# Kernel tuning notes

Hardware: AMD Instinct MI355X
Metric: run time of the kernel (lower is better)

Reference implementation:

```python
import jax, jax.numpy as jnp
import numpy as np

N = 25000          # nodes
E = 400000         # edges (avg degree 16)
H = 64             # hidden_nf
TYPE_DIM = 1
NL = 5             # 4 gcl layers + dgcl_0 (identical shapes, stacked)
GROUP = jnp.array([[[1., 0.], [0., 1.]], [[-1., 0.], [0., -1.]]], dtype=jnp.float32)  # [G,2,2]


def setup_inputs() -> dict:
    key = jax.random.key(0)
    ks = iter(jax.random.split(key, 40))
    def nrm(shape, scale=0.05):
        return jax.random.normal(next(ks), shape, dtype=jnp.float32) * scale
    inp = {}
    inp["nodes"] = nrm((N, 4 + TYPE_DIM), 1.0)
    inp["edges"] = jax.random.randint(next(ks), (2, E), 0, N)
    inp["edge_attr"] = nrm((E, 1), 1.0)
    # embedding: Linear(input_dim, H)
    inp["W_emb"] = nrm((4 + TYPE_DIM, H)); inp["b_emb"] = jnp.zeros((H,), jnp.float32)
    # group_mlp: Linear(G*H, H) -> SiLU -> Linear(H, H)
    G = GROUP.shape[0]
    inp["Wg1"] = nrm((G * H, H)); inp["bg1"] = jnp.zeros((H,), jnp.float32)
    inp["Wg2"] = nrm((H, H));     inp["bg2"] = jnp.zeros((H,), jnp.float32)
    # stacked GCL params for gcl_0..3 + dgcl_0 (all H->H, edges_in_nf=1)
    inp["eW1"] = nrm((NL, 2 * H + 1, H)); inp["eb1"] = jnp.zeros((NL, H), jnp.float32)
    inp["eW2"] = nrm((NL, H, H));         inp["eb2"] = jnp.zeros((NL, H), jnp.float32)
    inp["nW1"] = nrm((NL, 2 * H, H));     inp["nb1"] = jnp.zeros((NL, H), jnp.float32)
    inp["nW2"] = nrm((NL, H, H));         inp["nb2"] = jnp.zeros((NL, H), jnp.float32)
    # dgcl_1: GCL(H, 2*len(group)=4, H)
    inp["deW1"] = nrm((2 * H + 1, H)); inp["deb1"] = jnp.zeros((H,), jnp.float32)
    inp["deW2"] = nrm((H, H));         inp["deb2"] = jnp.zeros((H,), jnp.float32)
    inp["dnW1"] = nrm((2 * H, H));     inp["dnb1"] = jnp.zeros((H,), jnp.float32)
    inp["dnW2"] = nrm((H, 2 * G));     inp["dnb2"] = jnp.zeros((2 * G,), jnp.float32)
    return inp


def _gcl(h, row, col, edge_attr, eW1, eb1, eW2, eb2, nW1, nb1, nW2, nb2):
    # edge model: gather -> MLP (Linear,SiLU,Linear,SiLU)
    e_in = jnp.concatenate([h[row], h[col], edge_attr], axis=1)  # [E, 2H+1]
    e = jax.nn.silu(e_in @ eW1 + eb1)
    e = jax.nn.silu(e @ eW2 + eb2)                               # [E, H]
    # node model: scatter-sum by source index, then MLP (Linear,SiLU,Linear)
    agg = jax.ops.segment_sum(e, row, num_segments=h.shape[0])   # [N, H]
    out = jnp.concatenate([h, agg], axis=1)                      # [N, 2H]
    out = jax.nn.silu(out @ nW1 + nb1) @ nW2 + nb2
    return out  # recurrent=False: no residual


def reference(nodes, edges, edge_attr, W_emb, b_emb, Wg1, bg1, Wg2, bg2,
              eW1, eb1, eW2, eb2, nW1, nb1, nW2, nb2,
              deW1, deb1, deW2, deb2, dnW1, dnb1, dnW2, dnb2):
    loc, vel, ntype = nodes[:, :2], nodes[:, 2:4], nodes[:, 4:]
    # group-equivariant embedding: transform loc/vel by each group element
    loc_g = jnp.einsum('nd,gde->gne', loc, GROUP)   # [G, N, 2]
    vel_g = jnp.einsum('nd,gde->gne', vel, GROUP)   # [G, N, 2]
    ntype_g = jnp.broadcast_to(ntype, (GROUP.shape[0],) + ntype.shape)
    feats = jnp.concatenate([loc_g, vel_g, ntype_g], axis=2)   # [G, N, 5]
    h_g = feats @ W_emb + b_emb                                 # [G, N, H]
    h = jnp.transpose(h_g, (1, 0, 2)).reshape(nodes.shape[0], -1)  # [N, G*H]
    h = jax.nn.silu(h @ Wg1 + bg1) @ Wg2 + bg2
    row, col = edges[0], edges[1]
    for i in range(eW1.shape[0]):  # gcl_0..3 then dgcl_0
        h = _gcl(h, row, col, edge_attr, eW1[i], eb1[i], eW2[i], eb2[i],
                 nW1[i], nb1[i], nW2[i], nb2[i])
    # dgcl_1: node output dim = 2*len(group)
    x = _gcl(h, row, col, edge_attr, deW1, deb1, deW2, deb2,
             dnW1, dnb1, dnW2, dnb2)
    return x
```

## Files before the change

kernel.cpp:

```cpp
#include <hip/hip_runtime.h>
#include <hip/hip_bf16.h>

#define N_NODES 25000
#define N_EDGES 400000
#define NB_SCAN ((N_NODES + 255) / 256)
#define EDGE_TILES (N_EDGES / 16)
#define TPW 2
#define EDGE_WAVES (EDGE_TILES / TPW)
#define EDGE_BLOCKS (EDGE_WAVES / 4)
#define NODE_TILES ((N_NODES + 15) / 16)
#define NODE_BLOCKS2 ((NODE_TILES + 1) / 2)

typedef __attribute__((ext_vector_type(8))) short short8;
typedef __attribute__((ext_vector_type(4))) float f32x4;

__device__ __forceinline__ float silu_f(float x) {
  return x * __builtin_amdgcn_rcpf(1.0f + __expf(-x));
}

__device__ __forceinline__ short f2bf_s(float x) {
  __hip_bfloat16 h = __float2bfloat16(x);
  return *reinterpret_cast<short*>(&h);
}
__device__ __forceinline__ float bf_s2f(short s) {
  __hip_bfloat16 h = *reinterpret_cast<__hip_bfloat16*>(&s);
  return __bfloat162float(h);
}

__device__ __forceinline__ void load_afrag(const float* T, int s, int quad, int n16,
                                           short8& ahi, short8& alo) {
#pragma unroll
  for (int j = 0; j < 8; ++j) {
    float tv = T[(s * 32 + quad * 8 + j) * 17 + n16];
    short hi = f2bf_s(tv);
    ahi[j] = hi;
    alo[j] = f2bf_s(tv - bf_s2f(hi));
  }
}
__device__ __forceinline__ void load_bfrag(const float* __restrict__ W, int k0, int col,
                                           short8& bhi, short8& blo) {
#pragma unroll
  for (int j = 0; j < 8; ++j) {
    float w = W[(k0 + j) * 64 + col];
    short hi = f2bf_s(w);
    bhi[j] = hi;
    blo[j] = f2bf_s(w - bf_s2f(hi));
  }
}
__device__ __forceinline__ f32x4 mfma3(short8 ahi, short8 alo, short8 bhi, short8 blo,
                                       f32x4 acc) {
  acc = __builtin_amdgcn_mfma_f32_16x16x32_bf16(ahi, bhi, acc, 0, 0, 0);
  acc = __builtin_amdgcn_mfma_f32_16x16x32_bf16(ahi, blo, acc, 0, 0, 0);
  acc = __builtin_amdgcn_mfma_f32_16x16x32_bf16(alo, bhi, acc, 0, 0, 0);
  return acc;
}

__global__ __launch_bounds__(256) void k_hist(const int* __restrict__ rows,
                                              int* __restrict__ counts)
{
  int stride = gridDim.x * blockDim.x;
  for (int e = blockIdx.x * blockDim.x + threadIdx.x; e < N_EDGES; e += stride)
    atomicAdd(&counts[rows[e]], 1);
}

__global__ __launch_bounds__(256) void k_scanA(const int* __restrict__ counts,
                                               int* __restrict__ bsum)
{
  __shared__ int sd[256];
  int t = threadIdx.x;
  int i = blockIdx.x * 256 + t;
  int x = (i < N_NODES) ? counts[i] : 0;
  sd[t] = x; __syncthreads();
  for (int d = 128; d > 0; d >>= 1) { if (t < d) sd[t] += sd[t + d]; __syncthreads(); }
  if (t == 0) bsum[blockIdx.x] = sd[0];
}

__global__ __launch_bounds__(128) void k_scanB(const int* __restrict__ bsum,
                                               int* __restrict__ boffs)
{
  __shared__ int buf[128];
  int t = threadIdx.x;
  int x = (t < NB_SCAN) ? bsum[t] : 0;
  buf[t] = x; __syncthreads();
  for (int d = 1; d < 128; d <<= 1) {
    int y = (t >= d) ? buf[t - d] : 0;
    __syncthreads();
    buf[t] += y;
    __syncthreads();
  }
  if (t < NB_SCAN) boffs[t] = buf[t] - x;
}

__global__ __launch_bounds__(256) void k_scanC(const int* __restrict__ counts,
                                               const int* __restrict__ boffs,
                                               int* __restrict__ cursor)
{
  __shared__ int buf[256];
  int t = threadIdx.x;
  int i = blockIdx.x * 256 + t;
  int x = (i < N_NODES) ? counts[i] : 0;
  buf[t] = x; __syncthreads();
  for (int d = 1; d < 256; d <<= 1) {
    int y = (t >= d) ? buf[t - d] : 0;
    __syncthreads();
    buf[t] += y;
    __syncthreads();
  }
  if (i < N_NODES) cursor[i] = boffs[blockIdx.x] + buf[t] - x;
}

__global__ __launch_bounds__(256) void k_scatter(
    const int* __restrict__ rows, const int* __restrict__ cols,
    const float* __restrict__ eatt, int* __restrict__ cursor,
    int* __restrict__ srow, int* __restrict__ scol, float* __restrict__ sea)
{
  int stride = gridDim.x * blockDim.x;
  for (int e = blockIdx.x * blockDim.x + threadIdx.x; e < N_EDGES; e += stride) {
    int r = rows[e];
    int pos = atomicAdd(&cursor[r], 1);
    srow[pos] = r;
    scol[pos] = cols[e];
    sea[pos] = eatt[e];
  }
}

__global__ __launch_bounds__(256) void k_w2prep(const float* __restrict__ eW2,
                                                const float* __restrict__ deW2,
                                                short* __restrict__ w2p)
{
  int layer = blockIdx.x;
  const float* src = (layer < 5) ? (eW2 + layer * 64 * 64) : deW2;
  short* dst = w2p + layer * 8192;
  for (int t = threadIdx.x; t < 4096; t += 256) {
    int j = t & 7, n16 = (t >> 3) & 15, quad = (t >> 7) & 3, nt = (t >> 9) & 3,
        s = (t >> 11) & 1;
    float val = src[(s * 32 + quad * 8 + j) * 64 + nt * 16 + n16];
    short hi = f2bf_s(val);
    short lo = f2bf_s(val - bf_s2f(hi));
    int base = ((s * 4 + nt) * 4 + quad) * 128 + n16 * 8 + j;
    dst[base] = hi;
    dst[base + 4096] = lo;
  }
}

__global__ __launch_bounds__(256, 2) void k_embed_fused(
    const float* __restrict__ nodes,
    const float* __restrict__ W_emb, const float* __restrict__ b_emb,
    const float* __restrict__ Wg1, const float* __restrict__ bg1,
    const float* __restrict__ Wg2, const float* __restrict__ bg2,
    const float* __restrict__ eW1_0, const float* __restrict__ eb1_0,
    float* __restrict__ h, float* __restrict__ u, float* __restrict__ v,
    float* __restrict__ agg)
{
  const int lane = threadIdx.x & 63;
  const int wv = threadIdx.x >> 6;
  const int n16 = lane & 15;
  const int quad = lane >> 4;
  const int col = wv * 16 + n16;

  short8 W1hi[4], W1lo[4], W2hi[2], W2lo[2], Uhi[2], Ulo[2], Vhi[2], Vlo[2];
#pragma unroll
  for (int s = 0; s < 4; ++s)
    load_bfrag(Wg1, s * 32 + quad * 8, col, W1hi[s], W1lo[s]);
#pragma unroll
  for (int s = 0; s < 2; ++s) {
    load_bfrag(Wg2, s * 32 + quad * 8, col, W2hi[s], W2lo[s]);
    load_bfrag(eW1_0, s * 32 + quad * 8, col, Uhi[s], Ulo[s]);
    load_bfrag(eW1_0 + 64 * 64, s * 32 + quad * 8, col, Vhi[s], Vlo[s]);
  }
  float bg1v = bg1[col], bg2v = bg2[col], ebv = eb1_0[col];
  float w0 = W_emb[0 * 64 + lane], w1 = W_emb[1 * 64 + lane],
        w2 = W_emb[2 * 64 + lane], w3 = W_emb[3 * 64 + lane],
        w4 = W_emb[4 * 64 + lane];
  float bev = b_emb[lane];

  __shared__ float Ta[128 * 17];
  __shared__ float Tt[64 * 17];
  __shared__ float Th[64 * 17];
  __shared__ float Tu[64 * 17];
  __shared__ float Tv[64 * 17];

  int n0 = blockIdx.x * 16;
#pragma unroll
  for (int e4 = 0; e4 < 4; ++e4) {
    int e = wv * 4 + e4;
    int n = min(n0 + e, N_NODES - 1);
    float x0 = nodes[n * 5 + 0], x1 = nodes[n * 5 + 1],
          x2 = nodes[n * 5 + 2], x3 = nodes[n * 5 + 3],
          x4 = nodes[n * 5 + 4];
    float base = bev + x4 * w4;
    float sv = x0 * w0 + x1 * w1 + x2 * w2 + x3 * w3;
    Ta[lane * 17 + e] = base + sv;
    Ta[(64 + lane) * 17 + e] = base - sv;
  }
  __syncthreads();

  f32x4 a1 = {};
#pragma unroll
  for (int s = 0; s < 4; ++s) {
    short8 ahi, alo;
    load_afrag(Ta, s, quad, n16, ahi, alo);
    a1 = mfma3(ahi, alo, W1hi[s], W1lo[s], a1);
  }
#pragma unroll
  for (int r = 0; r < 4; ++r)
    Tt[col * 17 + quad * 4 + r] = silu_f(a1[r] + bg1v);
  __syncthreads();

  f32x4 a2 = {};
#pragma unroll
  for (int s = 0; s < 2; ++s) {
    short8 ahi, alo;
    load_afrag(Tt, s, quad, n16, ahi, alo);
    a2 = mfma3(ahi, alo, W2hi[s], W2lo[s], a2);
  }
#pragma unroll
  for (int r = 0; r < 4; ++r)
    Th[col * 17 + quad * 4 + r] = a2[r] + bg2v;
  __syncthreads();

  f32x4 aU = {}, aV = {};
#pragma unroll
  for (int s = 0; s < 2; ++s) {
    short8 ahi, alo;
    load_afrag(Th, s, quad, n16, ahi, alo);
    aU = mfma3(ahi, alo, Uhi[s], Ulo[s], aU);
    aV = mfma3(ahi, alo, Vhi[s], Vlo[s], aV);
  }
#pragma unroll
  for (int r = 0; r < 4; ++r) {
    Tu[col * 17 + quad * 4 + r] = aU[r] + ebv;
    Tv[col * 17 + quad * 4 + r] = aV[r];
  }
  __syncthreads();

#pragma unroll
  for (int e4 = 0; e4 < 4; ++e4) {
    int e = wv * 4 + e4;
    int n = n0 + e;
    if (n < N_NODES) {
      h[n * 64 + lane] = Th[lane * 17 + e];
      u[n * 64 + lane] = Tu[lane * 17 + e];
      v[n * 64 + lane] = Tv[lane * 17 + e];
      agg[n * 64 + lane] = 0.f;
    }
  }
}

__global__ __launch_bounds__(256, 2) void k_postfused(
    float* __restrict__ h, float* __restrict__ agg,
    const float* __restrict__ nW1, const float* __restrict__ nb1,
    const float* __restrict__ nW2, const float* __restrict__ nb2,
    const float* __restrict__ eW1n, const float* __restrict__ eb1n,
    float* __restrict__ u, float* __restrict__ v)
{
  const int lane = threadIdx.x & 63;
  const int wv = threadIdx.x >> 6;
  const int n16 = lane & 15;
  const int quad = lane >> 4;
  const int col = wv * 16 + n16;

  short8 W1hi[4], W1lo[4], W2hi[2], W2lo[2], Uhi[2], Ulo[2], Vhi[2], Vlo[2];
#pragma unroll
  for (int s = 0; s < 4; ++s)
    load_bfrag(nW1, s * 32 + quad * 8, col, W1hi[s], W1lo[s]);
#pragma unroll
  for (int s = 0; s < 2; ++s) {
    load_bfrag(nW2, s * 32 + quad * 8, col, W2hi[s], W2lo[s]);
    load_bfrag(eW1n, s * 32 + quad * 8, col, Uhi[s], Ulo[s]);
    load_bfrag(eW1n + 64 * 64, s * 32 + quad * 8, col, Vhi[s], Vlo[s]);
  }
  float b1 = nb1[col], b2 = nb2[col], ebv = eb1n[col];

  __shared__ float LA[2][128 * 17];
  __shared__ float LB[2][64 * 17];

  int t0 = blockIdx.x * 2;
#pragma unroll
  for (int q = 0; q < 2; ++q) {
    int n0 = (t0 + q) * 16;
#pragma unroll
    for (int e4 = 0; e4 < 4; ++e4) {
      int e = wv * 4 + e4;
      int n = min(n0 + e, N_NODES - 1);
      LA[q][lane * 17 + e] = h[n * 64 + lane];
      LA[q][(64 + lane) * 17 + e] = agg[n * 64 + lane];
    }
  }
  __syncthreads();

  f32x4 a1[2] = {};
#pragma unroll
  for (int q = 0; q < 2; ++q)
#pragma unroll
    for (int s = 0; s < 4; ++s) {
      short8 ahi, alo;
      load_afrag(LA[q], s, quad, n16, ahi, alo);
      a1[q] = mfma3(ahi, alo, W1hi[s], W1lo[s], a1[q]);
    }
#pragma unroll
  for (int q = 0; q < 2; ++q)
#pragma unroll
    for (int r = 0; r < 4; ++r)
      LB[q][col * 17 + quad * 4 + r] = silu_f(a1[q][r] + b1);
  __syncthreads();

  f32x4 a2[2] = {};
#pragma unroll
  for (int q = 0; q < 2; ++q)
#pragma unroll
    for (int s = 0; s < 2; ++s) {
      short8 ahi, alo;
      load_afrag(LB[q], s, quad, n16, ahi, alo);
      a2[q] = mfma3(ahi, alo, W2hi[s], W2lo[s], a2[q]);
    }
#pragma unroll
  for (int q = 0; q < 2; ++q)
#pragma unroll
    for (int r = 0; r < 4; ++r)
      LA[q][col * 17 + quad * 4 + r] = a2[q][r] + b2;
  __syncthreads();

  f32x4 aU[2] = {}, aV[2] = {};
#pragma unroll
  for (int q = 0; q < 2; ++q)
#pragma unroll
    for (int s = 0; s < 2; ++s) {
      short8 ahi, alo;
      load_afrag(LA[q], s, quad, n16, ahi, alo);
      aU[q] = mfma3(ahi, alo, Uhi[s], Ulo[s], aU[q]);
      aV[q] = mfma3(ahi, alo, Vhi[s], Vlo[s], aV[q]);
    }
#pragma unroll
  for (int q = 0; q < 2; ++q)
#pragma unroll
    for (int r = 0; r < 4; ++r) {
      LA[q][1088 + col * 17 + quad * 4 + r] = aU[q][r] + ebv;
      LB[q][col * 17 + quad * 4 + r] = aV[q][r];
    }
  __syncthreads();

#pragma unroll
  for (int q = 0; q < 2; ++q) {
    int n0 = (t0 + q) * 16;
#pragma unroll
    for (int e4 = 0; e4 < 4; ++e4) {
      int e = wv * 4 + e4;
      int n = n0 + e;
      if (n < N_NODES) {
        h[n * 64 + lane] = LA[q][lane * 17 + e];
        u[n * 64 + lane] = LA[q][1088 + lane * 17 + e];
        v[n * 64 + lane] = LB[q][lane * 17 + e];
        agg[n * 64 + lane] = 0.f;
      }
    }
  }
}

__global__ __launch_bounds__(256) void k_edge(
    const float* __restrict__ u, const float* __restrict__ v,
    const int* __restrict__ srow, const int* __restrict__ scol,
    const float* __restrict__ sea,
    const float* __restrict__ wea,
    const short* __restrict__ w2p, const float* __restrict__ eb2,
    float* __restrict__ agg)
{
  const int lane = threadIdx.x & 63;
  const int wv = threadIdx.x >> 6;
  const int n16 = lane & 15;
  const int quad = lane >> 4;

  const int wid = blockIdx.x * 4 + wv;
  const int tile0 = wid * TPW;
  int e0 = tile0 * 16;
  int e1 = e0 + 16;
  int rA = srow[e0 + n16], cA = scol[e0 + n16];
  int rB = srow[e1 + n16], cB = scol[e1 + n16];
  float eaA = sea[e0 + n16];
  float eaB = sea[e1 + n16];

  float4 weq[4];
  weq[0] = *reinterpret_cast<const float4*>(&wea[quad * 8]);
  weq[1] = *reinterpret_cast<const float4*>(&wea[quad * 8 + 4]);
  weq[2] = *reinterpret_cast<const float4*>(&wea[32 + quad * 8]);
  weq[3] = *reinterpret_cast<const float4*>(&wea[32 + quad * 8 + 4]);
  float b2v[4];
#pragma unroll
  for (int nt = 0; nt < 4; ++nt) b2v[nt] = eb2[nt * 16 + n16];

  auto gather_frag = [&](int r, int c, float4 (&uu)[4], float4 (&vv)[4]) {
    const float* ub = u + r * 64 + quad * 8;
    const float* vb = v + c * 64 + quad * 8;
    uu[0] = *reinterpret_cast<const float4*>(ub);
    uu[1] = *reinterpret_cast<const float4*>(ub + 4);
    uu[2] = *reinterpret_cast<const float4*>(ub + 32);
    uu[3] = *reinterpret_cast<const float4*>(ub + 36);
    vv[0] = *reinterpret_cast<const float4*>(vb);
    vv[1] = *reinterpret_cast<const float4*>(vb + 4);
    vv[2] = *reinterpret_cast<const float4*>(vb + 32);
    vv[3] = *reinterpret_cast<const float4*>(vb + 36);
  };

  float4 uuA[4], vvA[4];
  gather_frag(rA, cA, uuA, vvA);

  const short8* Wp8 = reinterpret_cast<const short8*>(w2p);
  short8 Whi[2][4], Wlo[2][4];
#pragma unroll
  for (int s = 0; s < 2; ++s)
#pragma unroll
    for (int nt = 0; nt < 4; ++nt) {
      Whi[s][nt] = Wp8[((s * 4 + nt) * 4 + quad) * 16 + n16];
      Wlo[s][nt] = Wp8[((s * 4 + nt) * 4 + quad) * 16 + n16 + 512];
    }

  int cur_row = -1;
  bool first_atomic = true;
  float asum[4] = {0.f, 0.f, 0.f, 0.f};

  auto reduce_pick = [&](float a0, float a1, float a2, float a3) -> float {
    a0 += __shfl_xor(a0, 16); a0 += __shfl_xor(a0, 32);
    a1 += __shfl_xor(a1, 16); a1 += __shfl_xor(a1, 32);
    a2 += __shfl_xor(a2, 16); a2 += __shfl_xor(a2, 32);
    a3 += __shfl_xor(a3, 16); a3 += __shfl_xor(a3, 32);
    float o = a0;
    o = (quad == 1) ? a1 : o;
    o = (quad == 2) ? a2 : o;
    o = (quad == 3) ? a3 : o;
    return o;
  };

  auto make_frags = [&](const float4 (&uu)[4], const float4 (&vv)[4], float ea,
                        short8 (&ahi)[2], short8 (&alo)[2]) {
    const float* uf = reinterpret_cast<const float*>(uu);
    const float* vf = reinterpret_cast<const float*>(vv);
    const float* wf = reinterpret_cast<const float*>(weq);
#pragma unroll
    for (int k = 0; k < 16; ++k) {
      float t = silu_f(uf[k] + vf[k] + ea * wf[k]);
      short hi = f2bf_s(t);
      ahi[k >> 3][k & 7] = hi;
      alo[k >> 3][k & 7] = f2bf_s(t - bf_s2f(hi));
    }
  };

  auto do_mfma = [&](const short8 (&ahi)[2], const short8 (&alo)[2], f32x4 (&acc)[4]) {
#pragma unroll
    for (int s = 0; s < 2; ++s)
#pragma unroll
      for (int nt = 0; nt < 4; ++nt) {
        acc[nt] = __builtin_amdgcn_mfma_f32_16x16x32_bf16(ahi[s], Whi[s][nt], acc[nt], 0, 0, 0);
        acc[nt] = __builtin_amdgcn_mfma_f32_16x16x32_bf16(ahi[s], Wlo[s][nt], acc[nt], 0, 0, 0);
        acc[nt] = __builtin_amdgcn_mfma_f32_16x16x32_bf16(alo[s], Whi[s][nt], acc[nt], 0, 0, 0);
      }
  };

  auto epilogue = [&](int r16a, f32x4 (&acc)[4]) {
    float ev[4][4];
#pragma unroll
    for (int reg = 0; reg < 4; ++reg)
#pragma unroll
      for (int nt = 0; nt < 4; ++nt)
        ev[reg][nt] = silu_f(acc[nt][reg] + b2v[nt]);

    int rup = __shfl_up(r16a, 1);
    bool nf = (lane < 16) && ((lane == 0) ? (r16a != cur_row) : (r16a != rup));
    unsigned mask = (unsigned)(__ballot(nf) & 0xFFFFull);

    int s = 0;
    while (s < 16) {
      if ((mask >> s) & 1u) {
        if (cur_row >= 0) {
          float o = reduce_pick(asum[0], asum[1], asum[2], asum[3]);
          if (first_atomic) { unsafeAtomicAdd(&agg[cur_row * 64 + lane], o); first_atomic = false; }
          else agg[cur_row * 64 + lane] = o;
        }
        asum[0] = asum[1] = asum[2] = asum[3] = 0.f;
        cur_row = __shfl(r16a, s);
      }
      unsigned rem = mask & ~((2u << s) - 1u);
      int e = rem ? (__ffs(rem) - 1) : 16;
#pragma unroll
      for (int reg = 0; reg < 4; ++reg) {
        int m = quad * 4 + reg;
        bool in = (m >= s) && (m < e);
        asum[0] += in ? ev[reg][0] : 0.f;
        asum[1] += in ? ev[reg][1] : 0.f;
        asum[2] += in ? ev[reg][2] : 0.f;
        asum[3] += in ? ev[reg][3] : 0.f;
      }
      s = e;
    }
  };

  short8 ahiA[2], aloA[2];
  make_frags(uuA, vvA, eaA, ahiA, aloA);
  float4 uuB[4], vvB[4];
  gather_frag(rB, cB, uuB, vvB);
  f32x4 accA[4] = {};
  do_mfma(ahiA, aloA, accA);
  epilogue(rA, accA);

  short8 ahiB[2], aloB[2];
  make_frags(uuB, vvB, eaB, ahiB, aloB);
  f32x4 accB[4] = {};
  do_mfma(ahiB, aloB, accB);
  epilogue(rB, accB);

  if (cur_row >= 0) {
    float o = reduce_pick(asum[0], asum[1], asum[2], asum[3]);
    unsafeAtomicAdd(&agg[cur_row * 64 + lane], o);
  }
}

__global__ __launch_bounds__(256, 2) void k_final_mfma(
    const float* __restrict__ h, const float* __restrict__ agg,
    const float* __restrict__ dnW1, const float* __restrict__ dnb1,
    const float* __restrict__ dnW2, const float* __restrict__ dnb2,
    float* __restrict__ out)
{
  const int lane = threadIdx.x & 63;
  const int wv = threadIdx.x >> 6;
  const int n16 = lane & 15;
  const int quad = lane >> 4;
  const int col = wv * 16 + n16;

  short8 W1hi[4], W1lo[4];
#pragma unroll
  for (int s = 0; s < 4; ++s)
    load_bfrag(dnW1, s * 32 + quad * 8, col, W1hi[s], W1lo[s]);
  float b1 = dnb1[col];

  __shared__ float Ta[128 * 17];
  __shared__ float Tt[64 * 17];
  __shared__ float W2s[256];
  __shared__ float Tp[4][64];

  W2s[threadIdx.x] = dnW2[threadIdx.x];

  int n0 = blockIdx.x * 16;
#pragma unroll
  for (int e4 = 0; e4 < 4; ++e4) {
    int e = wv * 4 + e4;
    int n = min(n0 + e, N_NODES - 1);
    Ta[lane * 17 + e] = h[n * 64 + lane];
    Ta[(64 + lane) * 17 + e] = agg[n * 64 + lane];
  }
  __syncthreads();

  f32x4 a1 = {};
#pragma unroll
  for (int s = 0; s < 4; ++s) {
    short8 ahi, alo;
    load_afrag(Ta, s, quad, n16, ahi, alo);
    a1 = mfma3(ahi, alo, W1hi[s], W1lo[s], a1);
  }
#pragma unroll
  for (int r = 0; r < 4; ++r)
    Tt[col * 17 + quad * 4 + r] = silu_f(a1[r] + b1);
  __syncthreads();

  int m = lane >> 2, c = lane & 3;
  float p = 0.f;
#pragma unroll
  for (int kk = 0; kk < 16; ++kk) {
    int k = wv * 16 + kk;
    p += Tt[k * 17 + m] * W2s[k * 4 + c];
  }
  Tp[wv][lane] = p;
  __syncthreads();

  if (threadIdx.x < 64) {
    int n = n0 + (threadIdx.x >> 2);
    if (n < N_NODES) {
      float o = Tp[0][threadIdx.x] + Tp[1][threadIdx.x] +
                Tp[2][threadIdx.x] + Tp[3][threadIdx.x] + dnb2[threadIdx.x & 3];
      out[n * 4 + (threadIdx.x & 3)] = o;
    }
  }
}

extern "C" void kernel_launch(void* const* d_in, const int* in_sizes, int n_in,
                              void* d_out, int out_size, void* d_ws, size_t ws_size,
                              hipStream_t stream)
{
  const float* nodes = (const float*)d_in[0];
  const int*   edges = (const int*)d_in[1];
  const float* eatt  = (const float*)d_in[2];
  const float* W_emb = (const float*)d_in[3];
  const float* b_emb = (const float*)d_in[4];
  const float* Wg1   = (const float*)d_in[5];
  const float* bg1   = (const float*)d_in[6];
  const float* Wg2   = (const float*)d_in[7];
  const float* bg2   = (const float*)d_in[8];
  const float* eW1   = (const float*)d_in[9];
  const float* eb1   = (const float*)d_in[10];
  const float* eW2   = (const float*)d_in[11];
  const float* eb2   = (const float*)d_in[12];
  const float* nW1   = (const float*)d_in[13];
  const float* nb1   = (const float*)d_in[14];
  const float* nW2   = (const float*)d_in[15];
  const float* nb2   = (const float*)d_in[16];
  const float* deW1  = (const float*)d_in[17];
  const float* deb1  = (const float*)d_in[18];
  const float* deW2  = (const float*)d_in[19];
  const float* deb2  = (const float*)d_in[20];
  const float* dnW1  = (const float*)d_in[21];
  const float* dnb1  = (const float*)d_in[22];
  const float* dnW2  = (const float*)d_in[23];
  const float* dnb2  = (const float*)d_in[24];
  float* out = (float*)d_out;

  float* h   = (float*)d_ws;
  float* u   = h + N_NODES * 64;
  float* v   = u + N_NODES * 64;
  float* agg = v + N_NODES * 64;
  int* counts = (int*)(agg + N_NODES * 64);
  int* cursor = counts + N_NODES;
  int* bsum   = cursor + N_NODES;
  int* boffs  = bsum + 128;
  int* srow   = boffs + 128;
  int* scol   = srow + N_EDGES;
  float* sea  = (float*)(scol + N_EDGES);
  short* w2p  = (short*)(sea + N_EDGES);

  const int* rows = edges;
  const int* cols = edges + N_EDGES;

  hipMemsetAsync(counts, 0, N_NODES * sizeof(int), stream);
  k_w2prep<<<6, 256, 0, stream>>>(eW2, deW2, w2p);
  k_hist<<<400, 256, 0, stream>>>(rows, counts);
  k_scanA<<<NB_SCAN, 256, 0, stream>>>(counts, bsum);
  k_scanB<<<1, 128, 0, stream>>>(bsum, boffs);
  k_scanC<<<NB_SCAN, 256, 0, stream>>>(counts, boffs, cursor);
  k_scatter<<<400, 256, 0, stream>>>(rows, cols, eatt, cursor, srow, scol, sea);

  k_embed_fused<<<NODE_TILES, 256, 0, stream>>>(nodes, W_emb, b_emb, Wg1, bg1,
                                                Wg2, bg2, eW1, eb1, h, u, v, agg);

  for (int i = 0; i < 5; ++i) {
    k_edge<<<EDGE_BLOCKS, 256, 0, stream>>>(u, v, srow, scol, sea,
                                            eW1 + i * 129 * 64 + 128 * 64,
                                            w2p + i * 8192, eb2 + i * 64, agg);
    const float* eW1next = (i < 4) ? (eW1 + (i + 1) * 129 * 64) : deW1;
    const float* eb1next = (i < 4) ? (eb1 + (i + 1) * 64) : deb1;
    k_postfused<<<NODE_BLOCKS2, 256, 0, stream>>>(h, agg,
                                                  nW1 + i * 128 * 64, nb1 + i * 64,
                                                  nW2 + i * 64 * 64, nb2 + i * 64,
                                                  eW1next, eb1next, u, v);
  }
  k_edge<<<EDGE_BLOCKS, 256, 0, stream>>>(u, v, srow, scol, sea, deW1 + 128 * 64,
                                          w2p + 5 * 8192, deb2, agg);
  k_final_mfma<<<NODE_TILES, 256, 0, stream>>>(h, agg, dnW1, dnb1, dnW2, dnb2, out);
}
```

Baseline: 508.0 us.

## Stage edge-MLP weights in LDS and raise k_edge occupancy target

The edge kernel now copies the packed bf16 second-layer weights and edge-attr weights into shared memory once per block and reads the MFMA B fragments from LDS inside the loop. Before, each lane held them in registers. The two edge tiles are processed in a sequential loop rather than a manually software-pipelined A/B schedule, and launch bounds request 8 blocks per CU. The aim is to cut register pressure so more waves can hide gather latency. In exchange it adds LDS traffic, a block barrier, and loses the explicit overlap of the second tile's gather with the first tile's compute.

Result: faster. 447.3 us (-11.9%).

```diff
diff --git a/kernel.cpp b/kernel.cpp
--- a/kernel.cpp
+++ b/kernel.cpp
@@ -357,7 +357,7 @@
   }
 }
 
-__global__ __launch_bounds__(256) void k_edge(
+__global__ __launch_bounds__(256, 8) void k_edge(
     const float* __restrict__ u, const float* __restrict__ v,
     const int* __restrict__ srow, const int* __restrict__ scol,
     const float* __restrict__ sea,
@@ -370,49 +370,25 @@
   const int n16 = lane & 15;
   const int quad = lane >> 4;
 
+  __shared__ short Wlds[8192];
+  __shared__ float weqlds[64];
+
+  {
+    const int4* s4 = reinterpret_cast<const int4*>(w2p);
+    int4* d4 = reinterpret_cast<int4*>(Wlds);
+    for (int i = threadIdx.x; i < 1024; i += 256) d4[i] = s4[i];
+    if (threadIdx.x < 64) weqlds[threadIdx.x] = wea[threadIdx.x];
+  }
+  __syncthreads();
+
+  const short8* WL = reinterpret_cast<const short8*>(Wlds);
+
+  float b2v[4];
+#pragma unroll
+  for (int nt = 0; nt < 4; ++nt) b2v[nt] = eb2[nt * 16 + n16];
+
   const int wid = blockIdx.x * 4 + wv;
   const int tile0 = wid * TPW;
-  int e0 = tile0 * 16;
-  int e1 = e0 + 16;
-  int rA = srow[e0 + n16], cA = scol[e0 + n16];
-  int rB = srow[e1 + n16], cB = scol[e1 + n16];
-  float eaA = sea[e0 + n16];
-  float eaB = sea[e1 + n16];
-
-  float4 weq[4];
-  weq[0] = *reinterpret_cast<const float4*>(&wea[quad * 8]);
-  weq[1] = *reinterpret_cast<const float4*>(&wea[quad * 8 + 4]);
-  weq[2] = *reinterpret_cast<const float4*>(&wea[32 + quad * 8]);
-  weq[3] = *reinterpret_cast<const float4*>(&wea[32 + quad * 8 + 4]);
-  float b2v[4];
-#pragma unroll
-  for (int nt = 0; nt < 4; ++nt) b2v[nt] = eb2[nt * 16 + n16];
-
-  auto gather_frag = [&](int r, int c, float4 (&uu)[4], float4 (&vv)[4]) {
-    const float* ub = u + r * 64 + quad * 8;
-    const float* vb = v + c * 64 + quad * 8;
-    uu[0] = *reinterpret_cast<const float4*>(ub);
-    uu[1] = *reinterpret_cast<const float4*>(ub + 4);
-    uu[2] = *reinterpret_cast<const float4*>(ub + 32);
-    uu[3] = *reinterpret_cast<const float4*>(ub + 36);
-    vv[0] = *reinterpret_cast<const float4*>(vb);
-    vv[1] = *reinterpret_cast<const float4*>(vb + 4);
-    vv[2] = *reinterpret_cast<const float4*>(vb + 32);
-    vv[3] = *reinterpret_cast<const float4*>(vb + 36);
-  };
-
-  float4 uuA[4], vvA[4];
-  gather_frag(rA, cA, uuA, vvA);
-
-  const short8* Wp8 = reinterpret_cast<const short8*>(w2p);
-  short8 Whi[2][4], Wlo[2][4];
-#pragma unroll
-  for (int s = 0; s < 2; ++s)
-#pragma unroll
-    for (int nt = 0; nt < 4; ++nt) {
-      Whi[s][nt] = Wp8[((s * 4 + nt) * 4 + quad) * 16 + n16];
-      Wlo[s][nt] = Wp8[((s * 4 + nt) * 4 + quad) * 16 + n16 + 512];
-    }
 
   int cur_row = -1;
   bool first_atomic = true;
@@ -428,31 +404,6 @@
     o = (quad == 2) ? a2 : o;
     o = (quad == 3) ? a3 : o;
     return o;
-  };
-
-  auto make_frags = [&](const float4 (&uu)[4], const float4 (&vv)[4], float ea,
-                        short8 (&ahi)[2], short8 (&alo)[2]) {
-    const float* uf = reinterpret_cast<const float*>(uu);
-    const float* vf = reinterpret_cast<const float*>(vv);
-    const float* wf = reinterpret_cast<const float*>(weq);
-#pragma unroll
-    for (int k = 0; k < 16; ++k) {
-      float t = silu_f(uf[k] + vf[k] + ea * wf[k]);
-      short hi = f2bf_s(t);
-      ahi[k >> 3][k & 7] = hi;
-      alo[k >> 3][k & 7] = f2bf_s(t - bf_s2f(hi));
-    }
-  };
-
-  auto do_mfma = [&](const short8 (&ahi)[2], const short8 (&alo)[2], f32x4 (&acc)[4]) {
-#pragma unroll
-    for (int s = 0; s < 2; ++s)
-#pragma unroll
-      for (int nt = 0; nt < 4; ++nt) {
-        acc[nt] = __builtin_amdgcn_mfma_f32_16x16x32_bf16(ahi[s], Whi[s][nt], acc[nt], 0, 0, 0);
-        acc[nt] = __builtin_amdgcn_mfma_f32_16x16x32_bf16(ahi[s], Wlo[s][nt], acc[nt], 0, 0, 0);
-        acc[nt] = __builtin_amdgcn_mfma_f32_16x16x32_bf16(alo[s], Whi[s][nt], acc[nt], 0, 0, 0);
-      }
   };
 
   auto epilogue = [&](int r16a, f32x4 (&acc)[4]) {
@@ -493,19 +444,58 @@
     }
   };
 
-  short8 ahiA[2], aloA[2];
-  make_frags(uuA, vvA, eaA, ahiA, aloA);
-  float4 uuB[4], vvB[4];
-  gather_frag(rB, cB, uuB, vvB);
-  f32x4 accA[4] = {};
-  do_mfma(ahiA, aloA, accA);
-  epilogue(rA, accA);
-
-  short8 ahiB[2], aloB[2];
-  make_frags(uuB, vvB, eaB, ahiB, aloB);
-  f32x4 accB[4] = {};
-  do_mfma(ahiB, aloB, accB);
-  epilogue(rB, accB);
+  for (int t = 0; t < TPW; ++t) {
+    int e0 = (tile0 + t) * 16;
+    int r16 = srow[e0 + n16];
+    int c16 = scol[e0 + n16];
+    float ea = sea[e0 + n16];
+
+    float4 uu[4], vv[4];
+    {
+      const float* ub = u + r16 * 64 + quad * 8;
+      const float* vb = v + c16 * 64 + quad * 8;
+      uu[0] = *reinterpret_cast<const float4*>(ub);
+      uu[1] = *reinterpret_cast<const float4*>(ub + 4);
+      uu[2] = *reinterpret_cast<const float4*>(ub + 32);
+      uu[3] = *reinterpret_cast<const float4*>(ub + 36);
+      vv[0] = *reinterpret_cast<const float4*>(vb);
+      vv[1] = *reinterpret_cast<const float4*>(vb + 4);
+      vv[2] = *reinterpret_cast<const float4*>(vb + 32);
+      vv[3] = *reinterpret_cast<const float4*>(vb + 36);
+    }
+
+    short8 ahi[2], alo[2];
+#pragma unroll
+    for (int g = 0; g < 4; ++g) {
+      int base = (g < 2) ? (quad * 8 + g * 4) : (32 + quad * 8 + (g - 2) * 4);
+      float4 wq = *reinterpret_cast<const float4*>(&weqlds[base]);
+      const float* uf = reinterpret_cast<const float*>(&uu[g]);
+      const float* vf = reinterpret_cast<const float*>(&vv[g]);
+      const float* wf = reinterpret_cast<const float*>(&wq);
+#pragma unroll
+      for (int j = 0; j < 4; ++j) {
+        int k = g * 4 + j;
+        float tv = silu_f(uf[j] + vf[j] + ea * wf[j]);
+        short hi = f2bf_s(tv);
+        ahi[k >> 3][k & 7] = hi;
+        alo[k >> 3][k & 7] = f2bf_s(tv - bf_s2f(hi));
+      }
+    }
+
+    f32x4 acc[4] = {};
+#pragma unroll
+    for (int s = 0; s < 2; ++s)
+#pragma unroll
+      for (int nt = 0; nt < 4; ++nt) {
+        short8 whi = WL[((s * 4 + nt) * 4 + quad) * 16 + n16];
+        short8 wlo = WL[((s * 4 + nt) * 4 + quad) * 16 + n16 + 512];
+        acc[nt] = __builtin_amdgcn_mfma_f32_16x16x32_bf16(ahi[s], whi, acc[nt], 0, 0, 0);
+        acc[nt] = __builtin_amdgcn_mfma_f32_16x16x32_bf16(ahi[s], wlo, acc[nt], 0, 0, 0);
+        acc[nt] = __builtin_amdgcn_mfma_f32_16x16x32_bf16(alo[s], whi, acc[nt], 0, 0, 0);
+      }
+
+    epilogue(r16, acc);
+  }
 
   if (cur_row >= 0) {
     float o = reduce_pick(asum[0], asum[1], asum[2], asum[3]);
```
